# Kernel tuning notes

Hardware: AMD Instinct MI355X
Metric: run time of the kernel (lower is better)

The kernel has to match this reference:

```python
import jax, jax.numpy as jnp
import numpy as np


def setup_inputs() -> dict:
    key = jax.random.key(0)
    ks = jax.random.split(key, 8)
    C = 256
    C8 = C // 8
    B, H, W = 8, 64, 64
    scale = 0.05
    return {
        "x": jax.random.normal(ks[0], (B, C, W, H), dtype=jnp.float32),
        "Wq": jax.random.normal(ks[1], (C8, C), dtype=jnp.float32) * scale,
        "bq": jax.random.normal(ks[2], (C8,), dtype=jnp.float32) * scale,
        "Wk": jax.random.normal(ks[3], (C8, C), dtype=jnp.float32) * scale,
        "bk": jax.random.normal(ks[4], (C8,), dtype=jnp.float32) * scale,
        "Wv": jax.random.normal(ks[5], (C, C), dtype=jnp.float32) * scale,
        "bv": jax.random.normal(ks[6], (C,), dtype=jnp.float32) * scale,
        "gamma": jax.random.normal(ks[7], (1,), dtype=jnp.float32),
    }


def reference(x, Wq, bq, Wk, bk, Wv, bv, gamma):
    B, C, W, H = x.shape
    N = W * H
    xf = x.reshape(B, C, N)  # flatten spatial dims: [B, C, N]
    # 1x1 convs == per-pixel channel matmuls
    q = jnp.einsum("oc,bcn->bno", Wq, xf) + bq  # [B, N, C/8]
    k = jnp.einsum("oc,bcn->bon", Wk, xf) + bk[None, :, None]  # [B, C/8, N]
    v = jnp.einsum("oc,bcn->bon", Wv, xf) + bv[None, :, None]  # [B, C, N]
    # unscaled QK^T softmax (dim=-1), as in the original
    attn = jax.nn.softmax(jnp.einsum("bno,bom->bnm", q, k), axis=-1)  # [B, N, N]
    # out[b,c,m] = sum_n v[b,c,n] * attn[b,m,n]
    out = jnp.einsum("bcn,bmn->bcm", v, attn).reshape(B, C, W, H)
    return gamma[0] * out + x
```

## Files before the change

### kernel.cpp

```cpp
#include <hip/hip_runtime.h>
#include <stdint.h>

#define B_ 8
#define C_ 256
#define N_ 4096

typedef __attribute__((ext_vector_type(8))) short short8;
typedef __attribute__((ext_vector_type(4))) float float4v;
typedef __attribute__((ext_vector_type(16))) float floatx16;

__device__ __forceinline__ uint16_t f2bfr(float f) {
  return (uint16_t)((__float_as_uint(f) + 0x8000u) >> 16);
}
__device__ __forceinline__ uint32_t pkbf(float lo, float hi) {
  return ((__float_as_uint(hi) + 0x8000u) & 0xffff0000u) |
         ((__float_as_uint(lo) + 0x8000u) >> 16);
}
__device__ __forceinline__ short8 ld8(const uint16_t* p) {
  union { ushort4 h[2]; short8 v; } u;
  u.h[0] = *reinterpret_cast<const ushort4*>(p);
  u.h[1] = *reinterpret_cast<const ushort4*>(p + 4);
  return u.v;
}

__global__ __launch_bounds__(256) void wconv_kernel(
    const float* __restrict__ Wq, const float* __restrict__ bq,
    const float* __restrict__ Wk, const float* __restrict__ bk,
    const float* __restrict__ Wv, const float* __restrict__ bv,
    uint16_t* __restrict__ Wc, float* __restrict__ bc)
{
  int tg = blockIdx.x * 256 + threadIdx.x;
  int idx = tg * 4;
  const float* src = (idx < 8192) ? (Wq + idx)
                   : (idx < 16384) ? (Wk + (idx - 8192))
                                   : (Wv + (idx - 16384));
  float4 wv = *reinterpret_cast<const float4*>(src);
  uint2 o;
  o.x = pkbf(wv.x, wv.y);
  o.y = pkbf(wv.z, wv.w);
  *reinterpret_cast<uint2*>(Wc + idx) = o;
  if (tg < 320) bc[tg] = (tg < 32) ? bq[tg] : (tg < 64) ? bk[tg - 32] : bv[tg - 64];
}

__global__ __launch_bounds__(512, 4) void qkv_mfma(
    const float* __restrict__ x, const uint16_t* __restrict__ Wc,
    const float* __restrict__ bc,
    uint16_t* __restrict__ Qw, uint16_t* __restrict__ Kw, uint16_t* __restrict__ Vw)
{
  __shared__ __align__(16) uint16_t xs[64][268];
  const int b = blockIdx.y, n0 = blockIdx.x * 64;
  const int tid = threadIdx.x;
  const int nl = tid & 63, grp = tid >> 6;
  const int w = grp, l15 = tid & 15, q = (tid & 63) >> 4;
  const int nb = w & 3;

  const float* xb = x + (size_t)b * C_ * N_ + n0;
  #pragma unroll
  for (int it = 0; it < 16; ++it) {
    int c2 = it * 16 + grp * 2;
    float f0 = xb[(size_t)c2 * N_ + nl];
    float f1 = xb[(size_t)(c2 + 1) * N_ + nl];
    *reinterpret_cast<uint32_t*>(&xs[nl][c2]) = pkbf(f0, f1);
  }
  __syncthreads();

  float4v acc[10];
  #pragma unroll
  for (int i = 0; i < 10; ++i) acc[i] = (float4v){0.f, 0.f, 0.f, 0.f};

  const int ob0 = (w >> 2) * 10;
  #pragma unroll
  for (int h2 = 0; h2 < 2; ++h2) {
    short8 bx[4];
    #pragma unroll
    for (int kb = 0; kb < 4; ++kb)
      bx[kb] = ld8(&xs[nb * 16 + l15][h2 * 128 + kb * 32 + q * 8]);
    #pragma unroll
    for (int oi = 0; oi < 10; ++oi) {
      int ob = ob0 + oi;
      const uint16_t* wr = Wc + (size_t)(ob * 16 + l15) * 256 + h2 * 128 + q * 8;
      short8 aw[4];
      #pragma unroll
      for (int kb = 0; kb < 4; ++kb)
        aw[kb] = *reinterpret_cast<const short8*>(wr + kb * 32);
      #pragma unroll
      for (int kb = 0; kb < 4; ++kb)
        acc[oi] = __builtin_amdgcn_mfma_f32_16x16x32_bf16(aw[kb], bx[kb], acc[oi], 0, 0, 0);
    }
  }

  __syncthreads();
  uint16_t (*qs)[72] = reinterpret_cast<uint16_t(*)[72]>(&xs[0][0]);
  if (w < 4) {
    #pragma unroll
    for (int oi = 0; oi < 4; ++oi) {
      float4v a = acc[oi];
      const float* bb = bc + oi * 16 + q * 4;
      uint2 pk2;
      pk2.x = pkbf(a.x + bb[0], a.y + bb[1]);
      pk2.y = pkbf(a.z + bb[2], a.w + bb[3]);
      *reinterpret_cast<uint2*>(&qs[nb * 16 + l15][oi * 16 + q * 4]) = pk2;
    }
  }
  __syncthreads();
  if (tid < 256) {
    int n = tid >> 2, sub = tid & 3;
    const uint16_t* row = qs[n];
    uint4 d0 = *reinterpret_cast<const uint4*>(&row[sub * 16]);
    uint4 d1 = *reinterpret_cast<const uint4*>(&row[sub * 16 + 8]);
    size_t nn = (size_t)b * N_ + n0 + n;
    if (sub < 2) {
      uint4* dst = reinterpret_cast<uint4*>(Qw + nn * 32 + sub * 16);
      dst[0] = d0; dst[1] = d1;
    } else {
      uint4* dst = reinterpret_cast<uint4*>(Kw + nn * 32 + (sub - 2) * 16);
      dst[0] = d0; dst[1] = d1;
    }
  }
  const size_t blk = ((size_t)b * 64 + blockIdx.x) * 4;
  const int half = l15 >> 3, j = l15 & 7;
  #pragma unroll
  for (int oi = 0; oi < 10; ++oi) {
    int ob = ob0 + oi;
    if (ob < 4) continue;
    float4v a = acc[oi];
    const float* bb = bc + ob * 16 + q * 4;
    int cb = ob * 16 - 64 + q * 4;
    size_t vaddr = (blk + (cb >> 6)) * 4096
                 + (size_t)(nb * 1024 + ((cb >> 5) & 1) * 512 + half * 256
                            + (cb & 31) * 8 + j);
    Vw[vaddr     ] = f2bfr(a.x + bb[0]);
    Vw[vaddr +  8] = f2bfr(a.y + bb[1]);
    Vw[vaddr + 16] = f2bfr(a.z + bb[2]);
    Vw[vaddr + 24] = f2bfr(a.w + bb[3]);
  }
}

__global__ __launch_bounds__(512, 4) void attn_mfma(
    const uint16_t* __restrict__ Qw, const uint16_t* __restrict__ Kw,
    const uint16_t* __restrict__ Vw, const float* __restrict__ x,
    const float* __restrict__ gamma, float* __restrict__ out)
{
  __shared__ __align__(16) union Smem {
    uint16_t Ps[2][64 * 76];
    float Os[128 * 69];
  } sm;
  __shared__ float Ls[64];

  const int b = blockIdx.y, m0 = blockIdx.x * 64;
  const int tid = threadIdx.x;
  const int w = tid >> 6, lane = tid & 63;
  const int l15 = lane & 15, q = lane >> 4;
  const int l31 = lane & 31, half = lane >> 5;
  const int nb = w & 3, mbp = (w >> 2) * 2;

  const uint16_t* Kb = Kw + (size_t)b * N_ * 32 + (size_t)(nb * 16 + l15) * 32 + q * 8;
  const short8 qf0 = *reinterpret_cast<const short8*>(
      Qw + ((size_t)b * N_ + m0 + (mbp    ) * 16 + l15) * 32 + q * 8);
  const short8 qf1 = *reinterpret_cast<const short8*>(
      Qw + ((size_t)b * N_ + m0 + (mbp + 1) * 16 + l15) * 32 + q * 8);
  const uint16_t* Vb = Vw + ((size_t)b * 64 * 4 + (w >> 1)) * 4096
                     + (w & 1) * 512 + half * 256 + l31 * 8;

  floatx16 O[2];
  #pragma unroll
  for (int i = 0; i < 16; ++i) { O[0][i] = 0.f; O[1][i] = 0.f; }
  float rs0 = 0.f, rs1 = 0.f;
  const float4v zero4 = (float4v){0.f, 0.f, 0.f, 0.f};
  if (tid < 64) Ls[tid] = 0.f;

  {
    short8 kf = *reinterpret_cast<const short8*>(Kb);
    float4v s0 = __builtin_amdgcn_mfma_f32_16x16x32_bf16(kf, qf0, zero4, 0, 0, 0);
    float4v s1 = __builtin_amdgcn_mfma_f32_16x16x32_bf16(kf, qf1, zero4, 0, 0, 0);
    float p0 = __expf(s0.x), p1 = __expf(s0.y), p2 = __expf(s0.z), p3 = __expf(s0.w);
    rs0 += (p0 + p1) + (p2 + p3);
    uint2 pw; pw.x = pkbf(p0, p1); pw.y = pkbf(p2, p3);
    *reinterpret_cast<uint2*>(&sm.Ps[0][((mbp)*16 + l15) * 76 + nb * 16 + q * 4]) = pw;
    float r0 = __expf(s1.x), r1 = __expf(s1.y), r2 = __expf(s1.z), r3 = __expf(s1.w);
    rs1 += (r0 + r1) + (r2 + r3);
    uint2 rw; rw.x = pkbf(r0, r1); rw.y = pkbf(r2, r3);
    *reinterpret_cast<uint2*>(&sm.Ps[0][((mbp + 1)*16 + l15) * 76 + nb * 16 + q * 4]) = rw;
  }
  __syncthreads();

  for (int t = 0; t < 64; ++t) {
    const int buf = t & 1;

    short8 kf;
    if (t < 63)
      kf = *reinterpret_cast<const short8*>(Kb + (size_t)(t + 1) * 64 * 32);
    short8 vf[4];
    const uint16_t* vt = Vb + (size_t)t * 16384;
    #pragma unroll
    for (int ks = 0; ks < 4; ++ks)
      vf[ks] = *reinterpret_cast<const short8*>(vt + ks * 1024);

    if (t < 63) {
      float4v s0 = __builtin_amdgcn_mfma_f32_16x16x32_bf16(kf, qf0, zero4, 0, 0, 0);
      float4v s1 = __builtin_amdgcn_mfma_f32_16x16x32_bf16(kf, qf1, zero4, 0, 0, 0);
      float p0 = __expf(s0.x), p1 = __expf(s0.y), p2 = __expf(s0.z), p3 = __expf(s0.w);
      rs0 += (p0 + p1) + (p2 + p3);
      uint2 pw; pw.x = pkbf(p0, p1); pw.y = pkbf(p2, p3);
      *reinterpret_cast<uint2*>(&sm.Ps[buf ^ 1][((mbp)*16 + l15) * 76 + nb * 16 + q * 4]) = pw;
      float r0 = __expf(s1.x), r1 = __expf(s1.y), r2 = __expf(s1.z), r3 = __expf(s1.w);
      rs1 += (r0 + r1) + (r2 + r3);
      uint2 rw; rw.x = pkbf(r0, r1); rw.y = pkbf(r2, r3);
      *reinterpret_cast<uint2*>(&sm.Ps[buf ^ 1][((mbp + 1)*16 + l15) * 76 + nb * 16 + q * 4]) = rw;
    }

    #pragma unroll
    for (int ks = 0; ks < 4; ++ks) {
      short8 pa0 = ld8(&sm.Ps[buf][(l31     ) * 76 + ks * 16 + half * 8]);
      short8 pa1 = ld8(&sm.Ps[buf][(32 + l31) * 76 + ks * 16 + half * 8]);
      O[0] = __builtin_amdgcn_mfma_f32_32x32x16_bf16(pa0, vf[ks], O[0], 0, 0, 0);
      O[1] = __builtin_amdgcn_mfma_f32_32x32x16_bf16(pa1, vf[ks], O[1], 0, 0, 0);
    }
    __syncthreads();
  }

  rs0 += __shfl_xor(rs0, 16); rs0 += __shfl_xor(rs0, 32);
  rs1 += __shfl_xor(rs1, 16); rs1 += __shfl_xor(rs1, 32);
  if (q == 0) {
    atomicAdd(&Ls[(mbp    ) * 16 + l15], rs0);
    atomicAdd(&Ls[(mbp + 1) * 16 + l15], rs1);
  }
  __syncthreads();
  if (tid < 64) Ls[tid] = gamma[0] / Ls[tid];
  __syncthreads();

  #pragma unroll
  for (int chunk = 0; chunk < 2; ++chunk) {
    if ((w >> 2) == chunk) {
      int cl = (w & 3) * 32 + l31;
      #pragma unroll
      for (int h = 0; h < 2; ++h)
        #pragma unroll
        for (int reg = 0; reg < 16; ++reg) {
          int m = h * 32 + (reg & 3) + 8 * (reg >> 2) + 4 * half;
          sm.Os[cl * 69 + m] = O[h][reg] * Ls[m];
        }
    }
    __syncthreads();
    {
      int cl = tid >> 2, msub = tid & 3;
      int c = chunk * 128 + cl;
      size_t idx = ((size_t)b * C_ + c) * N_ + m0 + msub * 16;
      const float* os = &sm.Os[cl * 69 + msub * 16];
      #pragma unroll
      for (int i = 0; i < 4; ++i) {
        float4 xv = *reinterpret_cast<const float4*>(x + idx + i * 4);
        float4 ov;
        ov.x = os[i * 4 + 0] + xv.x;
        ov.y = os[i * 4 + 1] + xv.y;
        ov.z = os[i * 4 + 2] + xv.z;
        ov.w = os[i * 4 + 3] + xv.w;
        *reinterpret_cast<float4*>(out + idx + i * 4) = ov;
      }
    }
    __syncthreads();
  }
}

extern "C" void kernel_launch(void* const* d_in, const int* in_sizes, int n_in,
                              void* d_out, int out_size, void* d_ws, size_t ws_size,
                              hipStream_t stream) {
  const float* x     = (const float*)d_in[0];
  const float* Wq    = (const float*)d_in[1];
  const float* bq    = (const float*)d_in[2];
  const float* Wk    = (const float*)d_in[3];
  const float* bk    = (const float*)d_in[4];
  const float* Wv    = (const float*)d_in[5];
  const float* bv    = (const float*)d_in[6];
  const float* gamma = (const float*)d_in[7];
  float* out = (float*)d_out;

  uint16_t* Qw = (uint16_t*)d_ws;
  uint16_t* Kw = Qw + (size_t)B_ * N_ * 32;
  uint16_t* Vw = Kw + (size_t)B_ * N_ * 32;
  uint16_t* Wc = Vw + (size_t)B_ * C_ * N_;
  float*    bc = (float*)(Wc + 320 * 256);

  wconv_kernel<<<80, 256, 0, stream>>>(Wq, bq, Wk, bk, Wv, bv, Wc, bc);
  dim3 grid(N_ / 64, B_), block(512);
  qkv_mfma<<<grid, block, 0, stream>>>(x, Wc, bc, Qw, Kw, Vw);
  attn_mfma<<<grid, block, 0, stream>>>(Qw, Kw, Vw, x, gamma, out);
}
```

Measured before the change: 230.4 us.

## Prefetch K/V a step ahead, hoist P loads, interleave batches in grid

In the attention loop, K fragments are now prefetched two steps ahead and V fragments one step ahead in registers, so global loads overlap the current step's MFMAs. LDS reads of P are hoisted before the score computation, and the PV MFMAs are wrapped in s_setprio. The grid is flattened so consecutive blocks cover different batches, which changes how work lands across CUs and L2. This uses more registers and may lower occupancy.

```diff
diff --git a/kernel.cpp b/kernel.cpp
--- a/kernel.cpp
+++ b/kernel.cpp
@@ -48,7 +48,9 @@
     uint16_t* __restrict__ Qw, uint16_t* __restrict__ Kw, uint16_t* __restrict__ Vw)
 {
   __shared__ __align__(16) uint16_t xs[64][268];
-  const int b = blockIdx.y, n0 = blockIdx.x * 64;
+  const int b = blockIdx.x & 7;
+  const int tile = blockIdx.x >> 3;
+  const int n0 = tile * 64;
   const int tid = threadIdx.x;
   const int nl = tid & 63, grp = tid >> 6;
   const int w = grp, l15 = tid & 15, q = (tid & 63) >> 4;
@@ -117,7 +119,7 @@
       dst[0] = d0; dst[1] = d1;
     }
   }
-  const size_t blk = ((size_t)b * 64 + blockIdx.x) * 4;
+  const size_t blk = ((size_t)b * 64 + tile) * 4;
   const int half = l15 >> 3, j = l15 & 7;
   #pragma unroll
   for (int oi = 0; oi < 10; ++oi) {
@@ -147,7 +149,8 @@
   } sm;
   __shared__ float Ls[64];
 
-  const int b = blockIdx.y, m0 = blockIdx.x * 64;
+  const int b = blockIdx.x & 7;
+  const int m0 = (blockIdx.x >> 3) * 64;
   const int tid = threadIdx.x;
   const int w = tid >> 6, lane = tid & 63;
   const int l15 = lane & 15, q = lane >> 4;
@@ -159,7 +162,7 @@
       Qw + ((size_t)b * N_ + m0 + (mbp    ) * 16 + l15) * 32 + q * 8);
   const short8 qf1 = *reinterpret_cast<const short8*>(
       Qw + ((size_t)b * N_ + m0 + (mbp + 1) * 16 + l15) * 32 + q * 8);
-  const uint16_t* Vb = Vw + ((size_t)b * 64 * 4 + (w >> 1)) * 4096
+  const uint16_t* Vb = Vw + ((size_t)b * 256 + (w >> 1)) * 4096
                      + (w & 1) * 512 + half * 256 + l31 * 8;
 
   floatx16 O[2];
@@ -169,10 +172,15 @@
   const float4v zero4 = (float4v){0.f, 0.f, 0.f, 0.f};
   if (tid < 64) Ls[tid] = 0.f;
 
+  short8 vc[4];
+  #pragma unroll
+  for (int ks = 0; ks < 4; ++ks)
+    vc[ks] = *reinterpret_cast<const short8*>(Vb + ks * 1024);
+  short8 k0 = *reinterpret_cast<const short8*>(Kb);
+  short8 kc = *reinterpret_cast<const short8*>(Kb + (size_t)64 * 32);
   {
-    short8 kf = *reinterpret_cast<const short8*>(Kb);
-    float4v s0 = __builtin_amdgcn_mfma_f32_16x16x32_bf16(kf, qf0, zero4, 0, 0, 0);
-    float4v s1 = __builtin_amdgcn_mfma_f32_16x16x32_bf16(kf, qf1, zero4, 0, 0, 0);
+    float4v s0 = __builtin_amdgcn_mfma_f32_16x16x32_bf16(k0, qf0, zero4, 0, 0, 0);
+    float4v s1 = __builtin_amdgcn_mfma_f32_16x16x32_bf16(k0, qf1, zero4, 0, 0, 0);
     float p0 = __expf(s0.x), p1 = __expf(s0.y), p2 = __expf(s0.z), p3 = __expf(s0.w);
     rs0 += (p0 + p1) + (p2 + p3);
     uint2 pw; pw.x = pkbf(p0, p1); pw.y = pkbf(p2, p3);
@@ -184,21 +192,31 @@
   }
   __syncthreads();
 
+  #pragma unroll 2
   for (int t = 0; t < 64; ++t) {
     const int buf = t & 1;
 
-    short8 kf;
-    if (t < 63)
-      kf = *reinterpret_cast<const short8*>(Kb + (size_t)(t + 1) * 64 * 32);
-    short8 vf[4];
-    const uint16_t* vt = Vb + (size_t)t * 16384;
-    #pragma unroll
-    for (int ks = 0; ks < 4; ++ks)
-      vf[ks] = *reinterpret_cast<const short8*>(vt + ks * 1024);
-
+    short8 vn[4];
     if (t < 63) {
-      float4v s0 = __builtin_amdgcn_mfma_f32_16x16x32_bf16(kf, qf0, zero4, 0, 0, 0);
-      float4v s1 = __builtin_amdgcn_mfma_f32_16x16x32_bf16(kf, qf1, zero4, 0, 0, 0);
+      const uint16_t* vt = Vb + (size_t)(t + 1) * 16384;
+      #pragma unroll
+      for (int ks = 0; ks < 4; ++ks)
+        vn[ks] = *reinterpret_cast<const short8*>(vt + ks * 1024);
+    }
+    short8 knext;
+    if (t < 62)
+      knext = *reinterpret_cast<const short8*>(Kb + (size_t)(t + 2) * 64 * 32);
+
+    short8 pa0[4], pa1[4];
+    #pragma unroll
+    for (int ks = 0; ks < 4; ++ks) {
+      pa0[ks] = ld8(&sm.Ps[buf][(l31     ) * 76 + ks * 16 + half * 8]);
+      pa1[ks] = ld8(&sm.Ps[buf][(32 + l31) * 76 + ks * 16 + half * 8]);
+    }
+
+    if (t < 63) {
+      float4v s0 = __builtin_amdgcn_mfma_f32_16x16x32_bf16(kc, qf0, zero4, 0, 0, 0);
+      float4v s1 = __builtin_amdgcn_mfma_f32_16x16x32_bf16(kc, qf1, zero4, 0, 0, 0);
       float p0 = __expf(s0.x), p1 = __expf(s0.y), p2 = __expf(s0.z), p3 = __expf(s0.w);
       rs0 += (p0 + p1) + (p2 + p3);
       uint2 pw; pw.x = pkbf(p0, p1); pw.y = pkbf(p2, p3);
@@ -209,14 +227,20 @@
       *reinterpret_cast<uint2*>(&sm.Ps[buf ^ 1][((mbp + 1)*16 + l15) * 76 + nb * 16 + q * 4]) = rw;
     }
 
+    __builtin_amdgcn_s_setprio(1);
     #pragma unroll
     for (int ks = 0; ks < 4; ++ks) {
-      short8 pa0 = ld8(&sm.Ps[buf][(l31     ) * 76 + ks * 16 + half * 8]);
-      short8 pa1 = ld8(&sm.Ps[buf][(32 + l31) * 76 + ks * 16 + half * 8]);
-      O[0] = __builtin_amdgcn_mfma_f32_32x32x16_bf16(pa0, vf[ks], O[0], 0, 0, 0);
-      O[1] = __builtin_amdgcn_mfma_f32_32x32x16_bf16(pa1, vf[ks], O[1], 0, 0, 0);
-    }
+      O[0] = __builtin_amdgcn_mfma_f32_32x32x16_bf16(pa0[ks], vc[ks], O[0], 0, 0, 0);
+      O[1] = __builtin_amdgcn_mfma_f32_32x32x16_bf16(pa1[ks], vc[ks], O[1], 0, 0, 0);
+    }
+    __builtin_amdgcn_s_setprio(0);
     __syncthreads();
+
+    if (t < 63) {
+      #pragma unroll
+      for (int ks = 0; ks < 4; ++ks) vc[ks] = vn[ks];
+    }
+    if (t < 62) kc = knext;
   }
 
   rs0 += __shfl_xor(rs0, 16); rs0 += __shfl_xor(rs0, 32);
@@ -282,7 +306,6 @@
   float*    bc = (float*)(Wc + 320 * 256);
 
   wconv_kernel<<<80, 256, 0, stream>>>(Wq, bq, Wk, bk, Wv, bv, Wc, bc);
-  dim3 grid(N_ / 64, B_), block(512);
-  qkv_mfma<<<grid, block, 0, stream>>>(x, Wc, bc, Qw, Kw, Vw);
-  attn_mfma<<<grid, block, 0, stream>>>(Qw, Kw, Vw, x, gamma, out);
-}
+  qkv_mfma<<<512, 512, 0, stream>>>(x, Wc, bc, Qw, Kw, Vw);
+  attn_mfma<<<512, 512, 0, stream>>>(Qw, Kw, Vw, x, gamma, out);
+}
```

Result: slower. 281.0 us (+21.9%).
